# Optimization experiments

Hardware: AMD Instinct MI355X
Metric: run time of the kernel (lower is better)

## Reference

```python
import jax, jax.numpy as jnp
import numpy as np

B, C, H, W = 4, 256, 64, 64
C8 = C // 8


def setup_inputs() -> dict:
    key = jax.random.key(0)
    ks = jax.random.split(key, 8)
    x = jax.random.normal(ks[0], (B, C, H, W), dtype=jnp.float32)
    # 1x1 conv weights act as per-pixel linear maps: [out_ch, in_ch]
    Wq = jax.random.normal(ks[1], (C8, C), dtype=jnp.float32) * 0.05
    bq = jax.random.normal(ks[2], (C8,), dtype=jnp.float32) * 0.01
    Wk = jax.random.normal(ks[3], (C8, C), dtype=jnp.float32) * 0.05
    bk = jax.random.normal(ks[4], (C8,), dtype=jnp.float32) * 0.01
    Wv = jax.random.normal(ks[5], (C, C), dtype=jnp.float32) * 0.05
    bv = jax.random.normal(ks[6], (C,), dtype=jnp.float32) * 0.01
    # torch inits gamma to 0 (identity); use nonzero so output exercises the attention path
    gamma = jnp.array(0.5, dtype=jnp.float32)
    return {"x": x, "Wq": Wq, "bq": bq, "Wk": Wk, "bk": bk, "Wv": Wv, "bv": bv, "gamma": gamma}


def reference(x, Wq, bq, Wk, bk, Wv, bv, gamma):
    b, c, h, w = x.shape
    n = h * w
    xf = x.reshape(b, c, n)                                   # [B,C,N]
    q = jnp.einsum('oc,bcn->bno', Wq, xf) + bq                # [B,N,C8] (proj_query permuted)
    k = jnp.einsum('oc,bcn->bon', Wk, xf) + bk[:, None]       # [B,C8,N]
    energy = jnp.einsum('bnc,bcm->bnm', q, k)                 # [B,N_q,N_k]
    # NOTE: torch Softmax(dim=1) -> normalize over the QUERY axis (axis=1)
    attention = jax.nn.softmax(energy, axis=1)
    v = jnp.einsum('oc,bcn->bon', Wv, xf) + bv[:, None]       # [B,C,N]
    out = jnp.einsum('bcn,bnm->bcm', v, attention).reshape(b, c, h, w)
    return gamma * out + x
```

## Files before the change

kernel.cpp:

```cpp
#include <hip/hip_runtime.h>
#include <hip/hip_bf16.h>

#define BN 4
#define CC 256
#define C8 32
#define NN 4096
#define PROJ_ROWS 320

typedef __attribute__((ext_vector_type(8))) short short8;
typedef __attribute__((ext_vector_type(4))) float f32x4;

__device__ __forceinline__ unsigned short f2bf(float f) {
    unsigned u = __builtin_bit_cast(unsigned, f);
    unsigned r = (u + 0x7fffu + ((u >> 16) & 1u)) >> 16;
    return (unsigned short)r;
}

__global__ __launch_bounds__(256) void proj_kernel(
    const float* __restrict__ x,
    const float* __restrict__ Wq, const float* __restrict__ bq,
    const float* __restrict__ Wk, const float* __restrict__ bk,
    const float* __restrict__ Wv, const float* __restrict__ bv,
    unsigned short* __restrict__ proj, unsigned short* __restrict__ qT)
{
    int bid = blockIdx.x;
    int b = bid >> 6, nt = bid & 63;
    int n0 = nt * 64;
    int tid = threadIdx.x;
    int w = tid >> 6, l = tid & 63, l15 = l & 15, lq = l >> 4;

    __shared__ alignas(16) unsigned short Xt[64][40];

    f32x4 acc[5][4];
#pragma unroll
    for (int gi = 0; gi < 5; gi++)
#pragma unroll
        for (int mi = 0; mi < 4; mi++) acc[gi][mi] = (f32x4){0.f, 0.f, 0.f, 0.f};

    int c_l = tid >> 3;
    int nb  = (tid & 7) * 8;

    for (int kc = 0; kc < 8; kc++) {
        __syncthreads();
        {
            const float* xp = x + ((size_t)(b * CC + kc * 32 + c_l)) * NN + n0 + nb;
            float4 x0 = *(const float4*)xp;
            float4 x1 = *(const float4*)(xp + 4);
            float t[8] = {x0.x, x0.y, x0.z, x0.w, x1.x, x1.y, x1.z, x1.w};
#pragma unroll
            for (int e = 0; e < 8; e++) Xt[nb + e][c_l] = f2bf(t[e]);
        }
        __syncthreads();

        float4 wf[5][2];
#pragma unroll
        for (int gi = 0; gi < 5; gi++) {
            int og = (w * 5 + gi) * 16 + l15;
            const float* wrow = (og < 32) ? (Wq + (size_t)og * CC)
                              : (og < 64) ? (Wk + (size_t)(og - 32) * CC)
                                          : (Wv + (size_t)(og - 64) * CC);
            const float* wp = wrow + kc * 32 + lq * 8;
            wf[gi][0] = *(const float4*)wp;
            wf[gi][1] = *(const float4*)(wp + 4);
        }
#pragma unroll
        for (int gi = 0; gi < 5; gi++) {
            unsigned short a8[8] __attribute__((aligned(16)));
            float tw[8] = {wf[gi][0].x, wf[gi][0].y, wf[gi][0].z, wf[gi][0].w,
                           wf[gi][1].x, wf[gi][1].y, wf[gi][1].z, wf[gi][1].w};
#pragma unroll
            for (int e = 0; e < 8; e++) a8[e] = f2bf(tw[e]);
            short8 af = *(const short8*)a8;
#pragma unroll
            for (int mi = 0; mi < 4; mi++) {
                short8 bf = *(const short8*)&Xt[mi * 16 + l15][lq * 8];
                acc[gi][mi] = __builtin_amdgcn_mfma_f32_16x16x32_bf16(af, bf, acc[gi][mi], 0, 0, 0);
            }
        }
    }

#pragma unroll
    for (int gi = 0; gi < 5; gi++) {
#pragma unroll
        for (int r = 0; r < 4; r++) {
            int og = (w * 5 + gi) * 16 + lq * 4 + r;
            float bias = (og < 32) ? bq[og] : (og < 64) ? bk[og - 32] : bv[og - 64];
#pragma unroll
            for (int mi = 0; mi < 4; mi++) {
                int n = n0 + mi * 16 + l15;
                unsigned short v16 = f2bf(acc[gi][mi][r] + bias);
                if (og < 32) {
                    qT[((size_t)b * NN + n) * C8 + og] = v16;
                } else {
                    proj[((size_t)b * PROJ_ROWS + og) * NN + n] = v16;
                }
            }
        }
    }
}

template<int NSPLIT, bool FINAL>
__global__ __launch_bounds__(256, 3) void attn_kernel(
    const unsigned short* __restrict__ proj,
    const unsigned short* __restrict__ qT,
    const float* __restrict__ x,
    const float* __restrict__ gamma_p,
    float* __restrict__ out,
    float* __restrict__ Opart,
    float* __restrict__ Lpart)
{
    constexpr int ITERS = 64 / NSPLIT;
    int bid = blockIdx.x;
    int h   = bid >> 8;
    int low = bid & 255;
    int xcd = low & 7;
    int b = xcd >> 1;
    int mtile = ((low >> 3) << 1) | (xcd & 1);
    int m0 = mtile * 64;
    int nbase = h * (ITERS * 64);

    int tid = threadIdx.x;
    int w = tid >> 6, l = tid & 63, l15 = l & 15, lq = l >> 4;

    __shared__ alignas(16) unsigned short ps[64][72];
    __shared__ float red[4][64];
    __shared__ float Ltot[64];

    const unsigned short* kbase = proj + ((size_t)b * PROJ_ROWS + C8) * NN;
    const unsigned short* vbase = proj + ((size_t)b * PROJ_ROWS + 64) * NN;
    const unsigned short* qbase = qT + (size_t)b * NN * C8;

    short8 kfrag[4];
#pragma unroll
    for (int mi = 0; mi < 4; mi++) {
        int col = m0 + mi * 16 + l15;
        unsigned short t8[8] __attribute__((aligned(16)));
#pragma unroll
        for (int j = 0; j < 8; j++)
            t8[j] = kbase[(size_t)(lq * 8 + j) * NN + col];
        kfrag[mi] = *(const short8*)t8;
    }

    f32x4 O[4][4];
#pragma unroll
    for (int ci = 0; ci < 4; ci++)
#pragma unroll
        for (int mi = 0; mi < 4; mi++) O[ci][mi] = (f32x4){0.f, 0.f, 0.f, 0.f};
    float runS[4] = {0.f, 0.f, 0.f, 0.f};

    short8 qfrag = *(const short8*)(qbase + (size_t)(nbase + 16 * w + l15) * C8 + lq * 8);
    f32x4 S[4];
#pragma unroll
    for (int mi = 0; mi < 4; mi++)
        S[mi] = __builtin_amdgcn_mfma_f32_16x16x32_bf16(
            qfrag, kfrag[mi], (f32x4){0.f, 0.f, 0.f, 0.f}, 0, 0, 0);

    for (int it = 0; it < ITERS; it++) {
        int n0c = nbase + it * 64;
        __syncthreads();
#pragma unroll
        for (int mi = 0; mi < 4; mi++) {
            float p0 = __expf(S[mi][0]);
            float p1 = __expf(S[mi][1]);
            float p2 = __expf(S[mi][2]);
            float p3 = __expf(S[mi][3]);
            runS[mi] += (p0 + p1) + (p2 + p3);
            unsigned pk0 = (unsigned)f2bf(p0) | ((unsigned)f2bf(p1) << 16);
            unsigned pk1 = (unsigned)f2bf(p2) | ((unsigned)f2bf(p3) << 16);
            *(uint2*)&ps[mi * 16 + l15][16 * w + lq * 4] = make_uint2(pk0, pk1);
        }
        __syncthreads();

        short8 qnext;
        if (it + 1 < ITERS)
            qnext = *(const short8*)(qbase + (size_t)(n0c + 64 + 16 * w + l15) * C8 + lq * 8);

#pragma unroll
        for (int kh = 0; kh < 2; kh++) {
            short8 av[4];
#pragma unroll
            for (int ci = 0; ci < 4; ci++)
                av[ci] = *(const short8*)(vbase
                         + (size_t)(64 * w + ci * 16 + l15) * NN + n0c + kh * 32 + lq * 8);
            short8 bfr[4];
#pragma unroll
            for (int mi = 0; mi < 4; mi++)
                bfr[mi] = *(const short8*)&ps[mi * 16 + l15][kh * 32 + lq * 8];
#pragma unroll
            for (int ci = 0; ci < 4; ci++)
#pragma unroll
                for (int mi = 0; mi < 4; mi++)
                    O[ci][mi] = __builtin_amdgcn_mfma_f32_16x16x32_bf16(
                        av[ci], bfr[mi], O[ci][mi], 0, 0, 0);
        }

        if (it + 1 < ITERS) {
            qfrag = qnext;
#pragma unroll
            for (int mi = 0; mi < 4; mi++)
                S[mi] = __builtin_amdgcn_mfma_f32_16x16x32_bf16(
                    qfrag, kfrag[mi], (f32x4){0.f, 0.f, 0.f, 0.f}, 0, 0, 0);
        }
    }

#pragma unroll
    for (int mi = 0; mi < 4; mi++) {
        float s = runS[mi];
        s += __shfl_xor(s, 16);
        s += __shfl_xor(s, 32);
        red[w][mi * 16 + l15] = s;
    }
    __syncthreads();
    if (tid < 64) Ltot[tid] = red[0][tid] + red[1][tid] + red[2][tid] + red[3][tid];
    __syncthreads();

    if constexpr (FINAL) {
        float gamma = gamma_p[0];
        float iv[4];
#pragma unroll
        for (int mi = 0; mi < 4; mi++) iv[mi] = 1.0f / Ltot[mi * 16 + l15];
#pragma unroll
        for (int ci = 0; ci < 4; ci++) {
#pragma unroll
            for (int mi = 0; mi < 4; mi++) {
                int m = m0 + mi * 16 + l15;
#pragma unroll
                for (int r = 0; r < 4; r++) {
                    int c = 64 * w + ci * 16 + lq * 4 + r;
                    size_t idx = ((size_t)b * CC + c) * NN + m;
                    out[idx] = gamma * (O[ci][mi][r] * iv[mi]) + x[idx];
                }
            }
        }
    } else {
        size_t p = ((size_t)h * BN + b) * 64 + mtile;
        if (tid < 64) Lpart[p * 64 + tid] = Ltot[tid];
        float* Ob = Opart + p * (size_t)(CC * 64);
#pragma unroll
        for (int ci = 0; ci < 4; ci++) {
#pragma unroll
            for (int mi = 0; mi < 4; mi++) {
#pragma unroll
                for (int r = 0; r < 4; r++) {
                    int c = 64 * w + ci * 16 + lq * 4 + r;
                    Ob[c * 64 + mi * 16 + l15] = O[ci][mi][r];
                }
            }
        }
    }
}

template<int NSPLIT>
__global__ __launch_bounds__(256) void combine_kernel(
    const float* __restrict__ Opart, const float* __restrict__ Lpart,
    const float* __restrict__ x, const float* __restrict__ gamma_p,
    float* __restrict__ out)
{
    int bid = blockIdx.x;
    int b = bid >> 6, mt = bid & 63;
    int tid = threadIdx.x;
    int m4 = tid & 15, c16 = tid >> 4;
    float gamma = gamma_p[0];

    f32x4 Ls = (f32x4){0.f, 0.f, 0.f, 0.f};
#pragma unroll
    for (int h = 0; h < NSPLIT; h++) {
        size_t p = ((size_t)h * BN + b) * 64 + mt;
        Ls += *(const f32x4*)(Lpart + p * 64 + m4 * 4);
    }
    f32x4 inv;
#pragma unroll
    for (int j = 0; j < 4; j++) inv[j] = 1.0f / Ls[j];

    for (int cp = 0; cp < 16; cp++) {
        int c = cp * 16 + c16;
        f32x4 acc = (f32x4){0.f, 0.f, 0.f, 0.f};
#pragma unroll
        for (int h = 0; h < NSPLIT; h++) {
            size_t p = ((size_t)h * BN + b) * 64 + mt;
            acc += *(const f32x4*)(Opart + p * (size_t)(CC * 64) + c * 64 + m4 * 4);
        }
        size_t idx = ((size_t)b * CC + c) * NN + mt * 64 + m4 * 4;
        f32x4 xv = *(const f32x4*)(x + idx);
        f32x4 o;
#pragma unroll
        for (int j = 0; j < 4; j++) o[j] = gamma * (acc[j] * inv[j]) + xv[j];
        *(f32x4*)(out + idx) = o;
    }
}

extern "C" void kernel_launch(void* const* d_in, const int* in_sizes, int n_in,
                              void* d_out, int out_size, void* d_ws, size_t ws_size,
                              hipStream_t stream) {
    const float* x     = (const float*)d_in[0];
    const float* Wq    = (const float*)d_in[1];
    const float* bq    = (const float*)d_in[2];
    const float* Wk    = (const float*)d_in[3];
    const float* bk    = (const float*)d_in[4];
    const float* Wv    = (const float*)d_in[5];
    const float* bv    = (const float*)d_in[6];
    const float* gamma = (const float*)d_in[7];
    float* out = (float*)d_out;
    (void)in_sizes; (void)n_in; (void)out_size;

    unsigned short* proj = (unsigned short*)d_ws;
    unsigned short* qT   = proj + (size_t)BN * PROJ_ROWS * NN;
    const size_t baseB = ((size_t)BN * PROJ_ROWS * NN + (size_t)BN * NN * C8) * 2;

    auto needB = [&](int ns) {
        size_t LpB = (size_t)ns * BN * 64 * 64 * 4;
        size_t OpB = (size_t)ns * BN * 64 * CC * 64 * 4;
        return baseB + LpB + OpB;
    };

    proj_kernel<<<256, 256, 0, stream>>>(x, Wq, bq, Wk, bk, Wv, bv, proj, qT);

    if (ws_size >= needB(4)) {
        float* Lpart = (float*)((char*)d_ws + baseB);
        float* Opart = Lpart + (size_t)4 * BN * 64 * 64;
        attn_kernel<4, false><<<1024, 256, 0, stream>>>(proj, qT, x, gamma, out, Opart, Lpart);
        combine_kernel<4><<<256, 256, 0, stream>>>(Opart, Lpart, x, gamma, out);
    } else if (ws_size >= needB(2)) {
        float* Lpart = (float*)((char*)d_ws + baseB);
        float* Opart = Lpart + (size_t)2 * BN * 64 * 64;
        attn_kernel<2, false><<<512, 256, 0, stream>>>(proj, qT, x, gamma, out, Opart, Lpart);
        combine_kernel<2><<<256, 256, 0, stream>>>(Opart, Lpart, x, gamma, out);
    } else {
        attn_kernel<1, true><<<256, 256, 0, stream>>>(proj, qT, x, gamma, out, nullptr, nullptr);
    }
}
```

Measured before the change: 196.4 us.

## Double-buffer softmax tile in attention and widen combine and projection staging

The attention kernel now double-buffers the exponentiated score tile in shared memory. The next tile's scores, exp and store are computed right after the current PV MFMAs, which removes one barrier per iteration and lets the exp work overlap MMA issue. Occupancy hint raised to 4 blocks per CU. The projection kernel stages all 256 input channels into LDS up front, replacing the per-chunk barrier pairs, at the cost of more shared memory per block. The combine kernel is split four ways over channels to launch more blocks.

```diff
diff --git a/kernel.cpp b/kernel.cpp
--- a/kernel.cpp
+++ b/kernel.cpp
@@ -29,29 +29,29 @@
     int tid = threadIdx.x;
     int w = tid >> 6, l = tid & 63, l15 = l & 15, lq = l >> 4;
 
-    __shared__ alignas(16) unsigned short Xt[64][40];
-
-    f32x4 acc[5][4];
-#pragma unroll
-    for (int gi = 0; gi < 5; gi++)
-#pragma unroll
-        for (int mi = 0; mi < 4; mi++) acc[gi][mi] = (f32x4){0.f, 0.f, 0.f, 0.f};
+    __shared__ alignas(16) unsigned short Xt[64][264];
 
     int c_l = tid >> 3;
     int nb  = (tid & 7) * 8;
 
+#pragma unroll
     for (int kc = 0; kc < 8; kc++) {
-        __syncthreads();
-        {
-            const float* xp = x + ((size_t)(b * CC + kc * 32 + c_l)) * NN + n0 + nb;
-            float4 x0 = *(const float4*)xp;
-            float4 x1 = *(const float4*)(xp + 4);
-            float t[8] = {x0.x, x0.y, x0.z, x0.w, x1.x, x1.y, x1.z, x1.w};
-#pragma unroll
-            for (int e = 0; e < 8; e++) Xt[nb + e][c_l] = f2bf(t[e]);
-        }
-        __syncthreads();
-
+        const float* xp = x + ((size_t)(b * CC + kc * 32 + c_l)) * NN + n0 + nb;
+        float4 x0 = *(const float4*)xp;
+        float4 x1 = *(const float4*)(xp + 4);
+        float t[8] = {x0.x, x0.y, x0.z, x0.w, x1.x, x1.y, x1.z, x1.w};
+#pragma unroll
+        for (int e = 0; e < 8; e++) Xt[nb + e][kc * 32 + c_l] = f2bf(t[e]);
+    }
+    __syncthreads();
+
+    f32x4 acc[5][4];
+#pragma unroll
+    for (int gi = 0; gi < 5; gi++)
+#pragma unroll
+        for (int mi = 0; mi < 4; mi++) acc[gi][mi] = (f32x4){0.f, 0.f, 0.f, 0.f};
+
+    for (int kc = 0; kc < 8; kc++) {
         float4 wf[5][2];
 #pragma unroll
         for (int gi = 0; gi < 5; gi++) {
@@ -73,7 +73,7 @@
             short8 af = *(const short8*)a8;
 #pragma unroll
             for (int mi = 0; mi < 4; mi++) {
-                short8 bf = *(const short8*)&Xt[mi * 16 + l15][lq * 8];
+                short8 bf = *(const short8*)&Xt[mi * 16 + l15][kc * 32 + lq * 8];
                 acc[gi][mi] = __builtin_amdgcn_mfma_f32_16x16x32_bf16(af, bf, acc[gi][mi], 0, 0, 0);
             }
         }
@@ -100,7 +100,7 @@
 }
 
 template<int NSPLIT, bool FINAL>
-__global__ __launch_bounds__(256, 3) void attn_kernel(
+__global__ __launch_bounds__(256, 4) void attn_kernel(
     const unsigned short* __restrict__ proj,
     const unsigned short* __restrict__ qT,
     const float* __restrict__ x,
@@ -122,7 +122,7 @@
     int tid = threadIdx.x;
     int w = tid >> 6, l = tid & 63, l15 = l & 15, lq = l >> 4;
 
-    __shared__ alignas(16) unsigned short ps[64][72];
+    __shared__ alignas(16) unsigned short ps[2][64][72];
     __shared__ float red[4][64];
     __shared__ float Ltot[64];
 
@@ -148,33 +148,28 @@
         for (int mi = 0; mi < 4; mi++) O[ci][mi] = (f32x4){0.f, 0.f, 0.f, 0.f};
     float runS[4] = {0.f, 0.f, 0.f, 0.f};
 
-    short8 qfrag = *(const short8*)(qbase + (size_t)(nbase + 16 * w + l15) * C8 + lq * 8);
-    f32x4 S[4];
-#pragma unroll
-    for (int mi = 0; mi < 4; mi++)
-        S[mi] = __builtin_amdgcn_mfma_f32_16x16x32_bf16(
-            qfrag, kfrag[mi], (f32x4){0.f, 0.f, 0.f, 0.f}, 0, 0, 0);
+    {
+        short8 qfrag = *(const short8*)(qbase + (size_t)(nbase + 16 * w + l15) * C8 + lq * 8);
+#pragma unroll
+        for (int mi = 0; mi < 4; mi++) {
+            f32x4 S = __builtin_amdgcn_mfma_f32_16x16x32_bf16(
+                qfrag, kfrag[mi], (f32x4){0.f, 0.f, 0.f, 0.f}, 0, 0, 0);
+            float p0 = __expf(S[0]);
+            float p1 = __expf(S[1]);
+            float p2 = __expf(S[2]);
+            float p3 = __expf(S[3]);
+            runS[mi] += (p0 + p1) + (p2 + p3);
+            unsigned pk0 = (unsigned)f2bf(p0) | ((unsigned)f2bf(p1) << 16);
+            unsigned pk1 = (unsigned)f2bf(p2) | ((unsigned)f2bf(p3) << 16);
+            *(uint2*)&ps[0][mi * 16 + l15][16 * w + lq * 4] = make_uint2(pk0, pk1);
+        }
+    }
 
     for (int it = 0; it < ITERS; it++) {
         int n0c = nbase + it * 64;
         __syncthreads();
-#pragma unroll
-        for (int mi = 0; mi < 4; mi++) {
-            float p0 = __expf(S[mi][0]);
-            float p1 = __expf(S[mi][1]);
-            float p2 = __expf(S[mi][2]);
-            float p3 = __expf(S[mi][3]);
-            runS[mi] += (p0 + p1) + (p2 + p3);
-            unsigned pk0 = (unsigned)f2bf(p0) | ((unsigned)f2bf(p1) << 16);
-            unsigned pk1 = (unsigned)f2bf(p2) | ((unsigned)f2bf(p3) << 16);
-            *(uint2*)&ps[mi * 16 + l15][16 * w + lq * 4] = make_uint2(pk0, pk1);
-        }
-        __syncthreads();
-
-        short8 qnext;
-        if (it + 1 < ITERS)
-            qnext = *(const short8*)(qbase + (size_t)(n0c + 64 + 16 * w + l15) * C8 + lq * 8);
-
+
+        const unsigned short* psrc = &ps[it & 1][0][0];
 #pragma unroll
         for (int kh = 0; kh < 2; kh++) {
             short8 av[4];
@@ -185,7 +180,7 @@
             short8 bfr[4];
 #pragma unroll
             for (int mi = 0; mi < 4; mi++)
-                bfr[mi] = *(const short8*)&ps[mi * 16 + l15][kh * 32 + lq * 8];
+                bfr[mi] = *(const short8*)(psrc + (mi * 16 + l15) * 72 + kh * 32 + lq * 8);
 #pragma unroll
             for (int ci = 0; ci < 4; ci++)
 #pragma unroll
@@ -195,11 +190,22 @@
         }
 
         if (it + 1 < ITERS) {
-            qfrag = qnext;
-#pragma unroll
-            for (int mi = 0; mi < 4; mi++)
-                S[mi] = __builtin_amdgcn_mfma_f32_16x16x32_bf16(
+            short8 qfrag = *(const short8*)(qbase
+                           + (size_t)(n0c + 64 + 16 * w + l15) * C8 + lq * 8);
+            unsigned short* pdst = &ps[(it + 1) & 1][0][0];
+#pragma unroll
+            for (int mi = 0; mi < 4; mi++) {
+                f32x4 S = __builtin_amdgcn_mfma_f32_16x16x32_bf16(
                     qfrag, kfrag[mi], (f32x4){0.f, 0.f, 0.f, 0.f}, 0, 0, 0);
+                float p0 = __expf(S[0]);
+                float p1 = __expf(S[1]);
+                float p2 = __expf(S[2]);
+                float p3 = __expf(S[3]);
+                runS[mi] += (p0 + p1) + (p2 + p3);
+                unsigned pk0 = (unsigned)f2bf(p0) | ((unsigned)f2bf(p1) << 16);
+                unsigned pk1 = (unsigned)f2bf(p2) | ((unsigned)f2bf(p3) << 16);
+                *(uint2*)(pdst + (mi * 16 + l15) * 72 + 16 * w + lq * 4) = make_uint2(pk0, pk1);
+            }
         }
     }
 
@@ -257,7 +263,9 @@
     float* __restrict__ out)
 {
     int bid = blockIdx.x;
-    int b = bid >> 6, mt = bid & 63;
+    int cq = bid & 3;
+    int mt = (bid >> 2) & 63;
+    int b  = bid >> 8;
     int tid = threadIdx.x;
     int m4 = tid & 15, c16 = tid >> 4;
     float gamma = gamma_p[0];
@@ -272,8 +280,9 @@
 #pragma unroll
     for (int j = 0; j < 4; j++) inv[j] = 1.0f / Ls[j];
 
-    for (int cp = 0; cp < 16; cp++) {
-        int c = cp * 16 + c16;
+#pragma unroll
+    for (int cp = 0; cp < 4; cp++) {
+        int c = cq * 64 + cp * 16 + c16;
         f32x4 acc = (f32x4){0.f, 0.f, 0.f, 0.f};
 #pragma unroll
         for (int h = 0; h < NSPLIT; h++) {
@@ -319,12 +328,12 @@
         float* Lpart = (float*)((char*)d_ws + baseB);
         float* Opart = Lpart + (size_t)4 * BN * 64 * 64;
         attn_kernel<4, false><<<1024, 256, 0, stream>>>(proj, qT, x, gamma, out, Opart, Lpart);
-        combine_kernel<4><<<256, 256, 0, stream>>>(Opart, Lpart, x, gamma, out);
+        combine_kernel<4><<<1024, 256, 0, stream>>>(Opart, Lpart, x, gamma, out);
     } else if (ws_size >= needB(2)) {
         float* Lpart = (float*)((char*)d_ws + baseB);
         float* Opart = Lpart + (size_t)2 * BN * 64 * 64;
         attn_kernel<2, false><<<512, 256, 0, stream>>>(proj, qT, x, gamma, out, Opart, Lpart);
-        combine_kernel<2><<<256, 256, 0, stream>>>(Opart, Lpart, x, gamma, out);
+        combine_kernel<2><<<1024, 256, 0, stream>>>(Opart, Lpart, x, gamma, out);
     } else {
         attn_kernel<1, true><<<256, 256, 0, stream>>>(proj, qT, x, gamma, out, nullptr, nullptr);
     }
```

After: 181.7 us. 1.08x faster.
